# Kernel optimization log

Hardware: AMD Instinct MI355X
Metric: run time of the kernel (lower is better)

## Reference

```python
import jax, jax.numpy as jnp
import numpy as np

N_NODES = 50000
N_GRAPHS = 100
NODES_PER_GRAPH = 500
N_EDGES = 800000
EMB = 128
N_LAYERS = 4
Z_DIM = 2 * EMB + 1  # [x_i, x_j, dist]
BN_EPS = 1e-5


def setup_inputs() -> dict:
    key = jax.random.key(0)
    ks = jax.random.split(key, 12)
    z = jax.random.randint(ks[0], (N_NODES,), 0, 100)
    pos = jax.random.normal(ks[1], (N_NODES, 3), dtype=jnp.float32) * 3.0
    batch = jnp.repeat(jnp.arange(N_GRAPHS), NODES_PER_GRAPH)
    # within-graph random edges (stands in for radius_graph's bounded-degree output)
    rng = np.random.default_rng(0)
    eg = np.repeat(np.arange(N_GRAPHS), N_EDGES // N_GRAPHS)
    src = eg * NODES_PER_GRAPH + rng.integers(0, NODES_PER_GRAPH, N_EDGES)
    dst = eg * NODES_PER_GRAPH + rng.integers(0, NODES_PER_GRAPH, N_EDGES)
    edge_index = jnp.asarray(np.stack([src, dst]), dtype=jnp.int64)
    s = 0.05
    emb = jax.random.normal(ks[2], (100, EMB), dtype=jnp.float32)
    Wf = jax.random.normal(ks[3], (N_LAYERS, Z_DIM, EMB), dtype=jnp.float32) * s
    bf = jnp.zeros((N_LAYERS, EMB), dtype=jnp.float32)
    Ws = jax.random.normal(ks[4], (N_LAYERS, Z_DIM, EMB), dtype=jnp.float32) * s
    bs = jnp.zeros((N_LAYERS, EMB), dtype=jnp.float32)
    bn1_g = jnp.ones((N_LAYERS, EMB), dtype=jnp.float32)
    bn1_b = jnp.zeros((N_LAYERS, EMB), dtype=jnp.float32)
    bn2_g = jnp.ones((N_LAYERS, EMB), dtype=jnp.float32)
    bn2_b = jnp.zeros((N_LAYERS, EMB), dtype=jnp.float32)
    W1 = jax.random.normal(ks[5], (EMB, EMB), dtype=jnp.float32) * s
    b1 = jnp.zeros((EMB,), dtype=jnp.float32)
    W2 = jax.random.normal(ks[6], (EMB, 1), dtype=jnp.float32) * s
    b2 = jnp.zeros((1,), dtype=jnp.float32)
    return {"pos": pos, "emb": emb, "Wf": Wf, "bf": bf, "Ws": Ws, "bs": bs,
            "bn1_g": bn1_g, "bn1_b": bn1_b, "bn2_g": bn2_g, "bn2_b": bn2_b,
            "W1": W1, "b1": b1, "W2": W2, "b2": b2,
            "z": z, "batch": batch, "edge_index": edge_index}


def _batchnorm(x, g, b):
    mu = jnp.mean(x, axis=0)
    var = jnp.var(x, axis=0)  # biased, matches torch BN training normalization
    return (x - mu) * jax.lax.rsqrt(var + BN_EPS) * g + b


def reference(pos, emb, Wf, bf, Ws, bs, bn1_g, bn1_b, bn2_g, bn2_b, W1, b1, W2, b2, z, batch, edge_index):
    j, i = edge_index[0], edge_index[1]  # source j -> target i (PyG flow)
    x = emb[z]  # [N, EMB]
    dist = jnp.linalg.norm(pos[i] - pos[j], axis=-1, keepdims=True)  # [E, 1]
    for l in range(N_LAYERS):
        zc = jnp.concatenate([x[i], x[j], dist], axis=-1)  # [E, 257]
        msg = jax.nn.sigmoid(zc @ Wf[l] + bf[l]) * jax.nn.softplus(zc @ Ws[l] + bs[l])
        agg = jax.ops.segment_sum(msg, i, num_segments=N_NODES)  # CGConv 'add' aggregation
        out = _batchnorm(agg, bn1_g[l], bn1_b[l]) + x  # CGConv internal BN + residual
        x = jax.nn.relu(_batchnorm(out, bn2_g[l], bn2_b[l]))  # outer BN + ReLU (dropout=0)
    # global mean pool over graphs
    gsum = jax.ops.segment_sum(x, batch, num_segments=N_GRAPHS)
    cnt = jax.ops.segment_sum(jnp.ones((N_NODES, 1), x.dtype), batch, num_segments=N_GRAPHS)
    g = gsum / cnt
    h = jax.nn.relu(g @ W1 + b1)
    return (h @ W2 + b2).reshape(-1)  # [N_GRAPHS]
```

## Files before the change

### kernel.cpp

```cpp
#include <hip/hip_runtime.h>

#define NN 50000
#define NG 100
#define NPG 500
#define NE 800000
#define EPG 8000
#define EMBD 128
#define NL 4
#define CS_BLOCKS 1000
#define CS_ROWS 50

typedef __attribute__((ext_vector_type(8))) short short8v;
typedef __attribute__((ext_vector_type(4))) float float4v;
typedef __attribute__((ext_vector_type(2))) float f2;

__device__ __forceinline__ unsigned short f2bf(float v) {
  unsigned u = __float_as_uint(v);
  u += 0x7FFFu + ((u >> 16) & 1u);
  return (unsigned short)(u >> 16);
}

__device__ __forceinline__ float fexp2(float x) {
#if __has_builtin(__builtin_amdgcn_exp2f)
  return __builtin_amdgcn_exp2f(x);
#else
  float r; asm("v_exp_f32 %0, %1" : "=v"(r) : "v"(x)); return r;
#endif
}
__device__ __forceinline__ float flog2(float x) {
#if __has_builtin(__builtin_amdgcn_logf)
  return __builtin_amdgcn_logf(x);
#else
  float r; asm("v_log_f32 %0, %1" : "=v"(r) : "v"(x)); return r;
#endif
}
__device__ __forceinline__ float frcp(float x) {
#if __has_builtin(__builtin_amdgcn_rcpf)
  return __builtin_amdgcn_rcpf(x);
#else
  float r; asm("v_rcp_f32 %0, %1" : "=v"(r) : "v"(x)); return r;
#endif
}

__device__ __forceinline__ f2 unpk(unsigned v) {
  f2 r;
  r.x = __uint_as_float(v << 16);
  r.y = __uint_as_float(v & 0xffff0000u);
  return r;
}

__global__ void prep_w(const float* __restrict__ Wf, const float* __restrict__ Ws,
                       unsigned short* __restrict__ whT) {
  int idx = blockIdx.x * 256 + threadIdx.x;
  int k = idx & 127;
  int oc = (idx >> 7) & 511;
  int l = idx >> 16;
  const float* W;
  int row, c;
  if (oc < 128) { W = Wf; row = k; c = oc; }
  else if (oc < 256) { W = Ws; row = k; c = oc - 128; }
  else {
    int t = oc - 256;
    int p = t >> 2, r = t & 3;
    c = 2 * p + (r & 1);
    W = (r < 2) ? Wf : Ws;
    row = 128 + k;
  }
  whT[idx] = f2bf(W[(size_t)l * 32896 + (size_t)row * 128 + c]);
}

__global__ void gather_x(const float* __restrict__ emb, const int* __restrict__ z,
                         float* __restrict__ x, unsigned short* __restrict__ xh) {
  const int total = NN * 32;
  for (int idx = blockIdx.x * 256 + threadIdx.x; idx < total; idx += gridDim.x * 256) {
    int n = idx >> 5, c4 = (idx & 31) * 4;
    float4 v = *(const float4*)(emb + (size_t)z[n] * EMBD + c4);
    size_t base = (size_t)idx * 4;
    *(float4*)(x + base) = v;
    ushort4 h;
    h.x = f2bf(v.x); h.y = f2bf(v.y); h.z = f2bf(v.z); h.w = f2bf(v.w);
    *(ushort4*)(xh + base) = h;
  }
}

__global__ __launch_bounds__(512) void csr_build(const int* __restrict__ ei,
                                                 const float* __restrict__ pos,
                                                 int* __restrict__ offs, int* __restrict__ deg,
                                                 uint2* __restrict__ csr) {
  __shared__ int hist[NPG];
  __shared__ int scan[512];
  const int g = blockIdx.x, t = threadIdx.x;
  const int nbase = g * NPG;
  const int e0 = g * EPG;
  for (int n = t; n < NPG; n += 512) hist[n] = 0;
  __syncthreads();
  for (int e = t; e < EPG; e += 512) atomicAdd(&hist[ei[NE + e0 + e] - nbase], 1);
  __syncthreads();
  int v = (t < NPG) ? hist[t] : 0;
  scan[t] = v;
  __syncthreads();
  for (int d = 1; d < 512; d <<= 1) {
    int a = (t >= d) ? scan[t - d] : 0;
    __syncthreads();
    scan[t] += a;
    __syncthreads();
  }
  if (t < NPG) {
    int off = scan[t] - v;
    offs[nbase + t] = e0 + off;
    deg[nbase + t] = v;
    hist[t] = off;
  }
  __syncthreads();
  for (int e = t; e < EPG; e += 512) {
    int j = ei[e0 + e];
    int i = ei[NE + e0 + e];
    float dx = pos[i * 3 + 0] - pos[j * 3 + 0];
    float dy = pos[i * 3 + 1] - pos[j * 3 + 1];
    float dz = pos[i * 3 + 2] - pos[j * 3 + 2];
    float dist = sqrtf(dx * dx + dy * dy + dz * dz);
    int p = atomicAdd(&hist[i - nbase], 1);
    csr[e0 + p] = make_uint2((unsigned)j, __float_as_uint(dist));
  }
}

#define BM 128
#define BN 128
__global__ __launch_bounds__(256, 2) void gemm_proj(const unsigned short* __restrict__ xh,
                                                    const unsigned short* __restrict__ whT,
                                                    unsigned short* __restrict__ P, int l) {
  __shared__ __align__(16) unsigned short smem[32768];
  unsigned short* sA = smem;
  unsigned short* sB = smem + 16384;
  const int tid = threadIdx.x;
  const int R0 = blockIdx.x * BM;
  const int C0 = blockIdx.y * BN;
  for (int gid = tid; gid < BM * 16; gid += 256) {
    int row = gid >> 4, gc = gid & 15;
    int grow = R0 + row;
    uint4 v = make_uint4(0u, 0u, 0u, 0u);
    if (grow < NN) v = *(const uint4*)(xh + (size_t)grow * 128 + gc * 8);
    int gs = (gc & 8) | ((gc ^ row) & 7);
    *(uint4*)((char*)sA + row * 256 + gs * 16) = v;
  }
  for (int gid = tid; gid < BN * 16; gid += 256) {
    int c = gid >> 4, gc = gid & 15;
    uint4 v = *(const uint4*)(whT + ((size_t)l * 512 + C0 + c) * 128 + gc * 8);
    int gs = (gc & 8) | ((gc ^ c) & 7);
    *(uint4*)((char*)sB + c * 256 + gs * 16) = v;
  }
  __syncthreads();
  const int w = tid >> 6, lane = tid & 63;
  const int lr = lane & 15, lk = lane >> 4;
  float4v acc[2][8];
#pragma unroll
  for (int i = 0; i < 2; i++)
#pragma unroll
    for (int j = 0; j < 8; j++) acc[i][j] = (float4v){0.f, 0.f, 0.f, 0.f};
#pragma unroll
  for (int kb = 0; kb < 4; kb++) {
    int g = kb * 4 + lk;
    short8v a[2], b[8];
#pragma unroll
    for (int rf = 0; rf < 2; rf++) {
      int row = w * 32 + rf * 16 + lr;
      int gs = (g & 8) | ((g ^ row) & 7);
      a[rf] = *(const short8v*)((const char*)sA + row * 256 + gs * 16);
    }
#pragma unroll
    for (int cf = 0; cf < 8; cf++) {
      int c = cf * 16 + lr;
      int gs = (g & 8) | ((g ^ c) & 7);
      b[cf] = *(const short8v*)((const char*)sB + c * 256 + gs * 16);
    }
#pragma unroll
    for (int rf = 0; rf < 2; rf++)
#pragma unroll
      for (int cf = 0; cf < 8; cf++)
        acc[rf][cf] = __builtin_amdgcn_mfma_f32_16x16x32_bf16(a[rf], b[cf], acc[rf][cf], 0, 0, 0);
  }
  __syncthreads();
  unsigned short* sC = smem;
#pragma unroll
  for (int rf = 0; rf < 2; rf++) {
#pragma unroll
    for (int cf = 0; cf < 8; cf++) {
      int col = cf * 16 + lr;
#pragma unroll
      for (int j = 0; j < 4; j++) {
        int row = w * 32 + rf * 16 + lk * 4 + j;
        sC[row * 136 + col] = f2bf(acc[rf][cf][j]);
      }
    }
  }
  __syncthreads();
  for (int it = tid; it < BM * 16; it += 256) {
    int row = it >> 4, gc = it & 15;
    int grow = R0 + row;
    if (grow < NN) {
      uint4 v = *(const uint4*)(sC + row * 136 + gc * 8);
      *(uint4*)(P + (size_t)grow * 512 + C0 + gc * 8) = v;
    }
  }
}

__global__ __launch_bounds__(256) void edge_gather(const unsigned short* __restrict__ P,
                                                   const uint2* __restrict__ csr,
                                                   const int* __restrict__ offs,
                                                   const int* __restrict__ deg,
                                                   const float* __restrict__ Wf,
                                                   const float* __restrict__ bf,
                                                   const float* __restrict__ Ws,
                                                   const float* __restrict__ bs,
                                                   float* __restrict__ agg, int l) {
  const float L = 1.4426950408889634f;
  const float LN2 = 0.6931471805599453f;
  const int lane = threadIdx.x & 63;
  const int wid = __builtin_amdgcn_readfirstlane(threadIdx.x >> 6);
  const int bid = blockIdx.x;
  const int xcd = bid & 7, bidx = bid >> 3;
  const int wg = (xcd < 4) ? xcd * 1563 + bidx : 4 * 1563 + (xcd - 4) * 1562 + bidx;
  const int i = wg * 4 + wid;
  const int f0 = lane * 2;

  const unsigned* Piu = (const unsigned*)(P + (size_t)i * 512);
  unsigned pif = Piu[lane];
  unsigned pis = Piu[64 + lane];

  float2 wfd = *(const float2*)(Wf + (size_t)l * 32896 + 256 * 128 + f0);
  float2 wsd = *(const float2*)(Ws + (size_t)l * 32896 + 256 * 128 + f0);
  float2 bfv = *(const float2*)(bf + l * 128 + f0);
  float2 bsv = *(const float2*)(bs + l * 128 + f0);

  f2 bflv, bslv, wflv, wslv;
  {
    f2 pi_f = unpk(pif), pi_s = unpk(pis);
    bflv.x = (pi_f.x + bfv.x) * L; bflv.y = (pi_f.y + bfv.y) * L;
    bslv.x = (pi_s.x + bsv.x) * L; bslv.y = (pi_s.y + bsv.y) * L;
    wflv.x = wfd.x * L; wflv.y = wfd.y * L;
    wslv.x = wsd.x * L; wslv.y = wsd.y * L;
  }

  const int off = __builtin_amdgcn_readfirstlane(offs[i]);
  const int nd = __builtin_amdgcn_readfirstlane(deg[i]);
  const uint2* ep = csr + off;
  f2 acc = (f2){0.f, 0.f};

#define EDGE_BODY(DVU, V)                                          \
  {                                                                \
    float dv = __uint_as_float(DVU);                               \
    f2 pf = unpk((V).x) * L + (bflv + dv * wflv);                  \
    f2 ps = unpk((V).y) * L + (bslv + dv * wslv);                  \
    f2 a, b, r, lg;                                                \
    a.x = fexp2(-pf.x); a.y = fexp2(-pf.y);                        \
    b.x = fexp2(ps.x);  b.y = fexp2(ps.y);                         \
    r.x = frcp(a.x + 1.f); r.y = frcp(a.y + 1.f);                  \
    lg.x = flog2(b.x + 1.f); lg.y = flog2(b.y + 1.f);              \
    acc += r * lg;                                                 \
  }

  int k = 0;
  for (; k + 3 < nd; k += 4) {
    uint2 ed = ep[k + (lane & 3)];
    unsigned j0 = __builtin_amdgcn_readlane(ed.x, 0);
    unsigned d0 = __builtin_amdgcn_readlane(ed.y, 0);
    unsigned j1 = __builtin_amdgcn_readlane(ed.x, 1);
    unsigned d1 = __builtin_amdgcn_readlane(ed.y, 1);
    unsigned j2 = __builtin_amdgcn_readlane(ed.x, 2);
    unsigned d2 = __builtin_amdgcn_readlane(ed.y, 2);
    unsigned j3 = __builtin_amdgcn_readlane(ed.x, 3);
    unsigned d3 = __builtin_amdgcn_readlane(ed.y, 3);
    uint2 v0 = ((const uint2*)(P + (size_t)j0 * 512))[64 + lane];
    uint2 v1 = ((const uint2*)(P + (size_t)j1 * 512))[64 + lane];
    uint2 v2 = ((const uint2*)(P + (size_t)j2 * 512))[64 + lane];
    uint2 v3 = ((const uint2*)(P + (size_t)j3 * 512))[64 + lane];
    EDGE_BODY(d0, v0)
    EDGE_BODY(d1, v1)
    EDGE_BODY(d2, v2)
    EDGE_BODY(d3, v3)
  }
  for (; k < nd; k++) {
    uint2 e0 = ep[k];
    unsigned j0 = __builtin_amdgcn_readfirstlane(e0.x);
    unsigned d0 = __builtin_amdgcn_readfirstlane(e0.y);
    uint2 v0 = ((const uint2*)(P + (size_t)j0 * 512))[64 + lane];
    EDGE_BODY(d0, v0)
  }
#undef EDGE_BODY

  acc.x *= LN2; acc.y *= LN2;
  *(f2*)(agg + (size_t)i * EMBD + f0) = acc;
}

__global__ __launch_bounds__(256) void col_stats(const float* __restrict__ agg,
                                                 const float* __restrict__ x,
                                                 float* __restrict__ partial) {
  const int b = blockIdx.x, tid = threadIdx.x;
  const int c4 = tid & 31;
  const int h = tid >> 5;
  const int r0 = b * CS_ROWS;
  float4 sa = {0, 0, 0, 0}, sa2 = {0, 0, 0, 0}, sx = {0, 0, 0, 0}, sx2 = {0, 0, 0, 0},
         sax = {0, 0, 0, 0};
  for (int rr = h; rr < CS_ROWS; rr += 8) {
    size_t idx = (size_t)(r0 + rr) * EMBD + c4 * 4;
    float4 a = *(const float4*)(agg + idx);
    float4 xv = *(const float4*)(x + idx);
    sa.x += a.x; sa.y += a.y; sa.z += a.z; sa.w += a.w;
    sa2.x += a.x * a.x; sa2.y += a.y * a.y; sa2.z += a.z * a.z; sa2.w += a.w * a.w;
    sx.x += xv.x; sx.y += xv.y; sx.z += xv.z; sx.w += xv.w;
    sx2.x += xv.x * xv.x; sx2.y += xv.y * xv.y; sx2.z += xv.z * xv.z; sx2.w += xv.w * xv.w;
    sax.x += a.x * xv.x; sax.y += a.y * xv.y; sax.z += a.z * xv.z; sax.w += a.w * xv.w;
  }
  __shared__ float4 sm[256];
  float* p = partial + (size_t)b * 640;
#define REDUCE_STAT(V, OUTOFF)                                              \
  sm[tid] = V;                                                              \
  __syncthreads();                                                          \
  if (h == 0) {                                                             \
    float4 s = sm[tid];                                                     \
    for (int g = 1; g < 8; g++) {                                           \
      float4 o = sm[g * 32 + tid];                                          \
      s.x += o.x; s.y += o.y; s.z += o.z; s.w += o.w;                       \
    }                                                                       \
    *(float4*)(p + (OUTOFF) + c4 * 4) = s;                                  \
  }                                                                         \
  __syncthreads();
  REDUCE_STAT(sa, 0)
  REDUCE_STAT(sa2, 128)
  REDUCE_STAT(sx, 256)
  REDUCE_STAT(sx2, 384)
  REDUCE_STAT(sax, 512)
#undef REDUCE_STAT
}

__global__ __launch_bounds__(256) void bn_fold(const float* __restrict__ partial,
                                               const float* __restrict__ bn1g,
                                               const float* __restrict__ bn1b,
                                               const float* __restrict__ bn2g,
                                               const float* __restrict__ bn2b,
                                               float* __restrict__ abc, int l) {
  __shared__ float sm[5 * 256];
  const int t = threadIdx.x;
  const int ci = t & 15;
  const int col = blockIdx.x * 16 + ci;
  const int chunk = t >> 4;
  float s0 = 0, s1 = 0, s2 = 0, s3 = 0, s4 = 0;
  for (int b = chunk; b < CS_BLOCKS; b += 16) {
    const float* p = partial + (size_t)b * 640 + col;
    s0 += p[0]; s1 += p[128]; s2 += p[256]; s3 += p[384]; s4 += p[512];
  }
  sm[t] = s0; sm[256 + t] = s1; sm[512 + t] = s2; sm[768 + t] = s3; sm[1024 + t] = s4;
  __syncthreads();
  if (t < 16) {
    int c = blockIdx.x * 16 + t;
    float a0 = 0, a1 = 0, a2 = 0, a3 = 0, a4 = 0;
    for (int ch = 0; ch < 16; ch++) {
      int u = ch * 16 + t;
      a0 += sm[u]; a1 += sm[256 + u]; a2 += sm[512 + u]; a3 += sm[768 + u]; a4 += sm[1024 + u];
    }
    const double Ninv = 1.0 / (double)NN;
    double Ea = a0 * Ninv, Ea2 = a1 * Ninv, Ex = a2 * Ninv, Ex2 = a3 * Ninv, Eax = a4 * Ninv;
    double var1 = Ea2 - Ea * Ea;
    double g1 = bn1g[l * 128 + c], b1 = bn1b[l * 128 + c];
    double g2 = bn2g[l * 128 + c], b2v = bn2b[l * 128 + c];
    double s1d = g1 / sqrt(var1 + 1e-5);
    double t1 = b1 - Ea * s1d;
    double mu_o = s1d * Ea + t1 + Ex;
    double Eo2 = s1d * s1d * Ea2 + 2.0 * s1d * t1 * Ea + t1 * t1 + 2.0 * (s1d * Eax + t1 * Ex) + Ex2;
    double var_o = Eo2 - mu_o * mu_o;
    double s2d = g2 / sqrt(var_o + 1e-5);
    double t2 = b2v - mu_o * s2d;
    abc[c] = (float)(s1d * s2d);
    abc[128 + c] = (float)s2d;
    abc[256 + c] = (float)(t1 * s2d + t2);
  }
}

__global__ void fuse_bn(const float* __restrict__ agg, float* __restrict__ x,
                        unsigned short* __restrict__ xh, const float* __restrict__ abc) {
  const int total = NN * 32;
  for (int idx = blockIdx.x * 256 + threadIdx.x; idx < total; idx += gridDim.x * 256) {
    int c4 = (idx & 31) * 4;
    size_t base = (size_t)idx * 4;
    float4 a = *(const float4*)(agg + base);
    float4 xv = *(const float4*)(x + base);
    float4 A = *(const float4*)(abc + c4);
    float4 B = *(const float4*)(abc + 128 + c4);
    float4 C = *(const float4*)(abc + 256 + c4);
    float4 o;
    o.x = fmaxf(fmaf(A.x, a.x, fmaf(B.x, xv.x, C.x)), 0.f);
    o.y = fmaxf(fmaf(A.y, a.y, fmaf(B.y, xv.y, C.y)), 0.f);
    o.z = fmaxf(fmaf(A.z, a.z, fmaf(B.z, xv.z, C.z)), 0.f);
    o.w = fmaxf(fmaf(A.w, a.w, fmaf(B.w, xv.w, C.w)), 0.f);
    *(float4*)(x + base) = o;
    ushort4 hh;
    hh.x = f2bf(o.x); hh.y = f2bf(o.y); hh.z = f2bf(o.z); hh.w = f2bf(o.w);
    *(ushort4*)(xh + base) = hh;
  }
}

__global__ __launch_bounds__(512) void pool_mlp(const float* __restrict__ x,
                                                const float* __restrict__ W1,
                                                const float* __restrict__ b1,
                                                const float* __restrict__ W2,
                                                const float* __restrict__ b2,
                                                float* __restrict__ out) {
  __shared__ float red[512];
  __shared__ float gl[128];
  const int g = blockIdx.x, t = threadIdx.x;
  const int c = t & 127, q = t >> 7;
  const float* bx = x + (size_t)g * NPG * EMBD;
  float s = 0.f;
  for (int r = q; r < NPG; r += 4) s += bx[(size_t)r * EMBD + c];
  red[t] = s;
  __syncthreads();
  if (q == 0) gl[c] = (red[c] + red[128 + c] + red[256 + c] + red[384 + c]) * (1.f / NPG);
  __syncthreads();
  float acc = 0.f;
  for (int k = q * 32; k < q * 32 + 32; k++) acc = fmaf(gl[k], W1[k * EMBD + c], acc);
  red[t] = acc;
  __syncthreads();
  if (q == 0) {
    float h = fmaxf(red[c] + red[128 + c] + red[256 + c] + red[384 + c] + b1[c], 0.f);
    red[c] = h * W2[c];
  }
  __syncthreads();
  for (int sft = 64; sft > 0; sft >>= 1) {
    if (t < sft) red[t] += red[t + sft];
    __syncthreads();
  }
  if (t == 0) out[g] = red[0] + b2[0];
}

extern "C" void kernel_launch(void* const* d_in, const int* in_sizes, int n_in,
                              void* d_out, int out_size, void* d_ws, size_t ws_size,
                              hipStream_t stream) {
  const float* pos = (const float*)d_in[0];
  const float* emb = (const float*)d_in[1];
  const float* Wf = (const float*)d_in[2];
  const float* bf = (const float*)d_in[3];
  const float* Ws = (const float*)d_in[4];
  const float* bs = (const float*)d_in[5];
  const float* bn1g = (const float*)d_in[6];
  const float* bn1b = (const float*)d_in[7];
  const float* bn2g = (const float*)d_in[8];
  const float* bn2b = (const float*)d_in[9];
  const float* W1 = (const float*)d_in[10];
  const float* b1 = (const float*)d_in[11];
  const float* W2 = (const float*)d_in[12];
  const float* b2 = (const float*)d_in[13];
  const int* z = (const int*)d_in[14];
  const int* ei = (const int*)d_in[16];
  float* out = (float*)d_out;

  char* ws = (char*)d_ws;
  float* x = (float*)(ws + 0);
  unsigned short* xh = (unsigned short*)(ws + 25600000);
  unsigned short* P = (unsigned short*)(ws + 38400000);
  float* agg = (float*)(ws + 89600000);
  uint2* csr = (uint2*)(ws + 115200000);
  int* deg = (int*)(ws + 121600000);
  int* offs = (int*)(ws + 121800000);
  unsigned short* whT = (unsigned short*)(ws + 122000000);
  float* partial = (float*)(ws + 122524288);
  float* abc = (float*)(ws + 125084288);

  prep_w<<<1024, 256, 0, stream>>>(Wf, Ws, whT);
  gather_x<<<2048, 256, 0, stream>>>(emb, z, x, xh);
  csr_build<<<NG, 512, 0, stream>>>(ei, pos, offs, deg, csr);
  for (int l = 0; l < NL; l++) {
    gemm_proj<<<dim3(391, 4), 256, 0, stream>>>(xh, whT, P, l);
    edge_gather<<<NN / 4, 256, 0, stream>>>(P, csr, offs, deg, Wf, bf, Ws, bs, agg, l);
    col_stats<<<CS_BLOCKS, 256, 0, stream>>>(agg, x, partial);
    bn_fold<<<8, 256, 0, stream>>>(partial, bn1g, bn1b, bn2g, bn2b, abc, l);
    fuse_bn<<<2048, 256, 0, stream>>>(agg, x, xh, abc);
  }
  pool_mlp<<<NG, 512, 0, stream>>>(x, W1, b1, W2, b2, out);
}
```

Measured before the change: 590.8 us.

## Drop fp32 node state, keep only bf16 features; widen edge batch to 8

Removes the fp32 copy of node features x and keeps only the bf16 copy, which col_stats, fuse_bn and pool_mlp now read and fuse_bn writes. This cuts that traffic from 16-byte to 8-byte loads and stores per four features, at the cost of bf16 rounding in the residual path and BN statistics. Separately, the edge_gather loop now loads 8 neighbor rows per iteration, with a clamped index and predication for the tail, replacing the 4-wide loop plus scalar remainder. This gives more memory-level parallelism per wave, at the cost of more registers.

```diff
diff --git a/kernel.cpp b/kernel.cpp
--- a/kernel.cpp
+++ b/kernel.cpp
@@ -18,6 +18,9 @@
   unsigned u = __float_as_uint(v);
   u += 0x7FFFu + ((u >> 16) & 1u);
   return (unsigned short)(u >> 16);
+}
+__device__ __forceinline__ float bf2f(unsigned short h) {
+  return __uint_as_float(((unsigned)h) << 16);
 }
 
 __device__ __forceinline__ float fexp2(float x) {
@@ -70,16 +73,14 @@
 }
 
 __global__ void gather_x(const float* __restrict__ emb, const int* __restrict__ z,
-                         float* __restrict__ x, unsigned short* __restrict__ xh) {
+                         unsigned short* __restrict__ xh) {
   const int total = NN * 32;
   for (int idx = blockIdx.x * 256 + threadIdx.x; idx < total; idx += gridDim.x * 256) {
     int n = idx >> 5, c4 = (idx & 31) * 4;
     float4 v = *(const float4*)(emb + (size_t)z[n] * EMBD + c4);
-    size_t base = (size_t)idx * 4;
-    *(float4*)(x + base) = v;
     ushort4 h;
     h.x = f2bf(v.x); h.y = f2bf(v.y); h.z = f2bf(v.z); h.w = f2bf(v.w);
-    *(ushort4*)(xh + base) = h;
+    *(ushort4*)(xh + (size_t)idx * 4) = h;
   }
 }
 
@@ -259,32 +260,24 @@
     acc += r * lg;                                                 \
   }
 
-  int k = 0;
-  for (; k + 3 < nd; k += 4) {
-    uint2 ed = ep[k + (lane & 3)];
-    unsigned j0 = __builtin_amdgcn_readlane(ed.x, 0);
-    unsigned d0 = __builtin_amdgcn_readlane(ed.y, 0);
-    unsigned j1 = __builtin_amdgcn_readlane(ed.x, 1);
-    unsigned d1 = __builtin_amdgcn_readlane(ed.y, 1);
-    unsigned j2 = __builtin_amdgcn_readlane(ed.x, 2);
-    unsigned d2 = __builtin_amdgcn_readlane(ed.y, 2);
-    unsigned j3 = __builtin_amdgcn_readlane(ed.x, 3);
-    unsigned d3 = __builtin_amdgcn_readlane(ed.y, 3);
-    uint2 v0 = ((const uint2*)(P + (size_t)j0 * 512))[64 + lane];
-    uint2 v1 = ((const uint2*)(P + (size_t)j1 * 512))[64 + lane];
-    uint2 v2 = ((const uint2*)(P + (size_t)j2 * 512))[64 + lane];
-    uint2 v3 = ((const uint2*)(P + (size_t)j3 * 512))[64 + lane];
-    EDGE_BODY(d0, v0)
-    EDGE_BODY(d1, v1)
-    EDGE_BODY(d2, v2)
-    EDGE_BODY(d3, v3)
-  }
-  for (; k < nd; k++) {
-    uint2 e0 = ep[k];
-    unsigned j0 = __builtin_amdgcn_readfirstlane(e0.x);
-    unsigned d0 = __builtin_amdgcn_readfirstlane(e0.y);
-    uint2 v0 = ((const uint2*)(P + (size_t)j0 * 512))[64 + lane];
-    EDGE_BODY(d0, v0)
+  for (int k = 0; k < nd; k += 8) {
+    const int rem = nd - k;
+    int le = lane & 7;
+    if (le >= rem) le = rem - 1;
+    uint2 ed = ep[k + le];
+    unsigned js[8], ds[8];
+#pragma unroll
+    for (int e = 0; e < 8; e++) {
+      js[e] = __builtin_amdgcn_readlane(ed.x, e);
+      ds[e] = __builtin_amdgcn_readlane(ed.y, e);
+    }
+    uint2 v[8];
+#pragma unroll
+    for (int e = 0; e < 8; e++)
+      v[e] = ((const uint2*)(P + (size_t)js[e] * 512))[64 + lane];
+#pragma unroll
+    for (int e = 0; e < 8; e++)
+      if (e < rem) EDGE_BODY(ds[e], v[e])
   }
 #undef EDGE_BODY
 
@@ -293,7 +286,7 @@
 }
 
 __global__ __launch_bounds__(256) void col_stats(const float* __restrict__ agg,
-                                                 const float* __restrict__ x,
+                                                 const unsigned short* __restrict__ xh,
                                                  float* __restrict__ partial) {
   const int b = blockIdx.x, tid = threadIdx.x;
   const int c4 = tid & 31;
@@ -304,12 +297,13 @@
   for (int rr = h; rr < CS_ROWS; rr += 8) {
     size_t idx = (size_t)(r0 + rr) * EMBD + c4 * 4;
     float4 a = *(const float4*)(agg + idx);
-    float4 xv = *(const float4*)(x + idx);
+    ushort4 hx = *(const ushort4*)(xh + idx);
+    float x0 = bf2f(hx.x), x1 = bf2f(hx.y), x2 = bf2f(hx.z), x3 = bf2f(hx.w);
     sa.x += a.x; sa.y += a.y; sa.z += a.z; sa.w += a.w;
     sa2.x += a.x * a.x; sa2.y += a.y * a.y; sa2.z += a.z * a.z; sa2.w += a.w * a.w;
-    sx.x += xv.x; sx.y += xv.y; sx.z += xv.z; sx.w += xv.w;
-    sx2.x += xv.x * xv.x; sx2.y += xv.y * xv.y; sx2.z += xv.z * xv.z; sx2.w += xv.w * xv.w;
-    sax.x += a.x * xv.x; sax.y += a.y * xv.y; sax.z += a.z * xv.z; sax.w += a.w * xv.w;
+    sx.x += x0; sx.y += x1; sx.z += x2; sx.w += x3;
+    sx2.x += x0 * x0; sx2.y += x1 * x1; sx2.z += x2 * x2; sx2.w += x3 * x3;
+    sax.x += a.x * x0; sax.y += a.y * x1; sax.z += a.z * x2; sax.w += a.w * x3;
   }
   __shared__ float4 sm[256];
   float* p = partial + (size_t)b * 640;
@@ -376,30 +370,29 @@
   }
 }
 
-__global__ void fuse_bn(const float* __restrict__ agg, float* __restrict__ x,
-                        unsigned short* __restrict__ xh, const float* __restrict__ abc) {
+__global__ void fuse_bn(const float* __restrict__ agg, unsigned short* __restrict__ xh,
+                        const float* __restrict__ abc) {
   const int total = NN * 32;
   for (int idx = blockIdx.x * 256 + threadIdx.x; idx < total; idx += gridDim.x * 256) {
     int c4 = (idx & 31) * 4;
     size_t base = (size_t)idx * 4;
     float4 a = *(const float4*)(agg + base);
-    float4 xv = *(const float4*)(x + base);
+    ushort4 hx = *(const ushort4*)(xh + base);
     float4 A = *(const float4*)(abc + c4);
     float4 B = *(const float4*)(abc + 128 + c4);
     float4 C = *(const float4*)(abc + 256 + c4);
     float4 o;
-    o.x = fmaxf(fmaf(A.x, a.x, fmaf(B.x, xv.x, C.x)), 0.f);
-    o.y = fmaxf(fmaf(A.y, a.y, fmaf(B.y, xv.y, C.y)), 0.f);
-    o.z = fmaxf(fmaf(A.z, a.z, fmaf(B.z, xv.z, C.z)), 0.f);
-    o.w = fmaxf(fmaf(A.w, a.w, fmaf(B.w, xv.w, C.w)), 0.f);
-    *(float4*)(x + base) = o;
+    o.x = fmaxf(fmaf(A.x, a.x, fmaf(B.x, bf2f(hx.x), C.x)), 0.f);
+    o.y = fmaxf(fmaf(A.y, a.y, fmaf(B.y, bf2f(hx.y), C.y)), 0.f);
+    o.z = fmaxf(fmaf(A.z, a.z, fmaf(B.z, bf2f(hx.z), C.z)), 0.f);
+    o.w = fmaxf(fmaf(A.w, a.w, fmaf(B.w, bf2f(hx.w), C.w)), 0.f);
     ushort4 hh;
     hh.x = f2bf(o.x); hh.y = f2bf(o.y); hh.z = f2bf(o.z); hh.w = f2bf(o.w);
     *(ushort4*)(xh + base) = hh;
   }
 }
 
-__global__ __launch_bounds__(512) void pool_mlp(const float* __restrict__ x,
+__global__ __launch_bounds__(512) void pool_mlp(const unsigned short* __restrict__ xh,
                                                 const float* __restrict__ W1,
                                                 const float* __restrict__ b1,
                                                 const float* __restrict__ W2,
@@ -409,9 +402,9 @@
   __shared__ float gl[128];
   const int g = blockIdx.x, t = threadIdx.x;
   const int c = t & 127, q = t >> 7;
-  const float* bx = x + (size_t)g * NPG * EMBD;
+  const unsigned short* bx = xh + (size_t)g * NPG * EMBD;
   float s = 0.f;
-  for (int r = q; r < NPG; r += 4) s += bx[(size_t)r * EMBD + c];
+  for (int r = q; r < NPG; r += 4) s += bf2f(bx[(size_t)r * EMBD + c]);
   red[t] = s;
   __syncthreads();
   if (q == 0) gl[c] = (red[c] + red[128 + c] + red[256 + c] + red[384 + c]) * (1.f / NPG);
@@ -454,26 +447,25 @@
   float* out = (float*)d_out;
 
   char* ws = (char*)d_ws;
-  float* x = (float*)(ws + 0);
-  unsigned short* xh = (unsigned short*)(ws + 25600000);
-  unsigned short* P = (unsigned short*)(ws + 38400000);
-  float* agg = (float*)(ws + 89600000);
-  uint2* csr = (uint2*)(ws + 115200000);
-  int* deg = (int*)(ws + 121600000);
-  int* offs = (int*)(ws + 121800000);
-  unsigned short* whT = (unsigned short*)(ws + 122000000);
-  float* partial = (float*)(ws + 122524288);
-  float* abc = (float*)(ws + 125084288);
+  unsigned short* xh = (unsigned short*)(ws + 0);
+  unsigned short* P = (unsigned short*)(ws + 12800000);
+  float* agg = (float*)(ws + 64000000);
+  uint2* csr = (uint2*)(ws + 89600000);
+  int* deg = (int*)(ws + 96000000);
+  int* offs = (int*)(ws + 96200000);
+  unsigned short* whT = (unsigned short*)(ws + 96400000);
+  float* partial = (float*)(ws + 96924288);
+  float* abc = (float*)(ws + 99484288);
 
   prep_w<<<1024, 256, 0, stream>>>(Wf, Ws, whT);
-  gather_x<<<2048, 256, 0, stream>>>(emb, z, x, xh);
+  gather_x<<<2048, 256, 0, stream>>>(emb, z, xh);
   csr_build<<<NG, 512, 0, stream>>>(ei, pos, offs, deg, csr);
   for (int l = 0; l < NL; l++) {
     gemm_proj<<<dim3(391, 4), 256, 0, stream>>>(xh, whT, P, l);
     edge_gather<<<NN / 4, 256, 0, stream>>>(P, csr, offs, deg, Wf, bf, Ws, bs, agg, l);
-    col_stats<<<CS_BLOCKS, 256, 0, stream>>>(agg, x, partial);
+    col_stats<<<CS_BLOCKS, 256, 0, stream>>>(agg, xh, partial);
     bn_fold<<<8, 256, 0, stream>>>(partial, bn1g, bn1b, bn2g, bn2b, abc, l);
-    fuse_bn<<<2048, 256, 0, stream>>>(agg, x, xh, abc);
-  }
-  pool_mlp<<<NG, 512, 0, stream>>>(x, W1, b1, W2, b2, out);
-}
+    fuse_bn<<<2048, 256, 0, stream>>>(agg, xh, abc);
+  }
+  pool_mlp<<<NG, 512, 0, stream>>>(xh, W1, b1, W2, b2, out);
+}
```

Measured after the change: 581.0 us. About the same (-1.7%).
